# Optimization experiments

Measured on AMD Instinct MI355X. Metric: run time of the kernel, lower is better.

Reference implementation:

```python
import jax, jax.numpy as jnp
import numpy as np

N = 100000          # nodes
E = 1600000         # edges
IN_DIM = 128
HID = 64
N_CLASSES = 40
N_GAT_LAYERS = 2    # n_layers - 1
ALPHA = 0.2         # LeakyReLU slope
NEG_BIG = -9.0e15


def setup_inputs() -> dict:
    key = jax.random.key(0)
    ks = jax.random.split(key, 8)
    x = jax.random.normal(ks[0], (N, IN_DIM), dtype=jnp.float32)
    edge_index = jax.random.randint(ks[1], (2, E), 0, N, dtype=jnp.int64)
    # parameters (xavier-ish scale)
    emb_w = jax.random.normal(ks[2], (IN_DIM, HID), dtype=jnp.float32) * (1.414 / np.sqrt(IN_DIM + HID))
    emb_b = jnp.zeros((HID,), dtype=jnp.float32)
    Ws = jax.random.normal(ks[3], (N_GAT_LAYERS, HID, HID), dtype=jnp.float32) * (1.414 / np.sqrt(2 * HID))
    attn_a = jax.random.normal(ks[4], (N_GAT_LAYERS, 1, 2 * HID), dtype=jnp.float32) * (1.414 / np.sqrt(1 + 2 * HID))
    out_w = jax.random.normal(ks[5], (HID, N_CLASSES), dtype=jnp.float32) * (1.414 / np.sqrt(HID + N_CLASSES))
    out_b = jnp.zeros((N_CLASSES,), dtype=jnp.float32)
    return {"x": x, "edge_index": edge_index, "emb_w": emb_w, "emb_b": emb_b,
            "Ws": Ws, "attn_a": attn_a, "out_w": out_w, "out_b": out_b}


def _gat_conv(x, edge_src, edge_dst, W, a):
    # x: [N, d_in], W: [d_in, d_out], a: [1, 2*d_out]
    wh = x @ W                                   # [N, d_out]
    d = wh.shape[1]
    a_src = a[0, :d]                             # [d]
    a_dst = a[0, d:]                             # [d]
    # (a * cat(wh[src], wh[dst])).sum(1) == (wh @ a_src)[src] + (wh @ a_dst)[dst]
    s_src = wh @ a_src                           # [N]
    s_dst = wh @ a_dst                           # [N]
    e = jax.nn.leaky_relu(s_src[edge_src] + s_dst[edge_dst], negative_slope=ALPHA)  # [E]
    att = jnp.where(e > 0, e, NEG_BIG)
    att = jax.nn.softmax(att, axis=0)            # GLOBAL softmax over all edges (as in source)
    # scatter-aggregate weighted neighbor features into destination nodes
    msgs = att[:, None] * wh[edge_src]           # [E, d_out]
    h_prime = jax.ops.segment_sum(msgs, edge_dst, num_segments=wh.shape[0])  # [N, d_out]
    return jax.nn.elu(h_prime)                   # concat=True branch


def reference(x, edge_index, emb_w, emb_b, Ws, attn_a, out_w, out_b):
    edge_src = edge_index[0]
    edge_dst = edge_index[1]
    h = x @ emb_w + emb_b                        # emb Linear
    for l in range(N_GAT_LAYERS):
        h = _gat_conv(h, edge_src, edge_dst, Ws[l], attn_a[l])
    h = h @ out_w + out_b                        # out_att Linear
    h = jax.nn.elu(h)
    return jax.nn.log_softmax(h, axis=1)
```

## Files before the change

kernel.cpp:

```cpp
#include <hip/hip_runtime.h>
#include <hip/hip_bf16.h>

#define NODES   100000
#define EDGES   1600000
#define INDIM   128
#define HID     64
#define NCLS    40
#define NEG_BIG_F (-9000000000000000.0f)
#define SENTINEL  (-3.0e38f)

#define BN       512
#define NBUCK    196
#define CHUNK    7168
#define NCHUNK   ((EDGES + CHUNK - 1) / CHUNK)
#define BCAP     8960
#define AGB      3125
#define SMB      128

using bf16x8 = __attribute__((ext_vector_type(8))) short;
using f32x4  = __attribute__((ext_vector_type(4))) float;

static __device__ __forceinline__ float b2f(__hip_bfloat16 h){
    return __bfloat162float(h);
}
static __device__ __forceinline__ float bits2f(unsigned int b){
    union { unsigned int u; float f; } v; v.u = b << 16; return v.f;
}
static __device__ __forceinline__ unsigned short f2b(float f){
    __hip_bfloat16 h = __float2bfloat16(f);
    return *reinterpret_cast<unsigned short*>(&h);
}
static __device__ __forceinline__ float ldin(const void* p, int i, bool f32){
    return f32 ? ((const float*)p)[i] : b2f(((const __hip_bfloat16*)p)[i]);
}
static __device__ __forceinline__ float elu_fast(float x){
    return (x > 0.f) ? x : (__expf(x) - 1.f);
}
static __device__ __forceinline__ unsigned fenc(float f){
    unsigned u = __float_as_uint(f);
    return (u & 0x80000000u) ? ~u : (u | 0x80000000u);
}
static __device__ __forceinline__ float fdec(unsigned k){
    return __uint_as_float((k & 0x80000000u) ? (k & 0x7fffffffu) : ~k);
}
static __device__ __forceinline__ int ld_src(const int* ei, int i, bool i64){
    return i64 ? ei[2*i] : ei[i];
}
static __device__ __forceinline__ int ld_dst(const int* ei, int i, bool i64){
    return i64 ? ei[2*(EDGES + i)] : ei[EDGES + i];
}

__global__ __launch_bounds__(256) void k_detect(const unsigned* __restrict__ xw,
                                                const unsigned* __restrict__ eiw,
                                                int* __restrict__ flags){
    __shared__ int s1[256], s2[256];
    int t = threadIdx.x;
    int c1 = 0, c2 = 0;
    for(int i = t; i < 1024; i += 256){
        unsigned e = (xw[i] >> 23) & 0xffu;
        c1 += (e >= 90u && e <= 160u) ? 1 : 0;
        c2 += (eiw[2*i + 1] == 0u) ? 1 : 0;
    }
    s1[t] = c1; s2[t] = c2; __syncthreads();
    for(int off = 128; off > 0; off >>= 1){
        if(t < off){ s1[t] += s1[t+off]; s2[t] += s2[t+off]; }
        __syncthreads();
    }
    if(t == 0){ flags[0] = (s1[0] > 512) ? 1 : 0; flags[1] = (s2[0] > 512) ? 1 : 0; }
}

__global__ __launch_bounds__(256) void k_bhist(const int* __restrict__ ei,
                                               const int* __restrict__ flags,
                                               int* __restrict__ bdeg){
    __shared__ int sh[NBUCK];
    bool i64 = flags[1] != 0;
    int t = threadIdx.x;
    for(int i = t; i < NBUCK; i += 256) sh[i] = 0;
    __syncthreads();
    int i = blockIdx.x*256 + t;
    int stride = gridDim.x*256;
    for(; i < EDGES; i += stride) atomicAdd(&sh[ld_dst(ei, i, i64) >> 9], 1);
    __syncthreads();
    for(int b = t; b < NBUCK; b += 256) if(sh[b]) atomicAdd(&bdeg[b], sh[b]);
}

__global__ __launch_bounds__(256) void k_bscan(const int* __restrict__ bdeg,
                        int* __restrict__ bstart, int* __restrict__ bcursor,
                        unsigned* __restrict__ maxk){
    __shared__ int sh[256];
    int t = threadIdx.x;
    int v = (t < NBUCK) ? bdeg[t] : 0;
    sh[t] = v; __syncthreads();
    for(int off = 1; off < 256; off <<= 1){
        int x = (t >= off) ? sh[t - off] : 0;
        __syncthreads();
        sh[t] += x;
        __syncthreads();
    }
    int excl = sh[t] - v;
    if(t < NBUCK){ bstart[t] = excl; bcursor[t] = excl; }
    if(t == 255) bstart[NBUCK] = sh[255];
    if(t == 0){ maxk[0] = 0u; maxk[1] = 0u; }
}

__global__ __launch_bounds__(256) void k_bucket_scatter(const int* __restrict__ ei,
    const int* __restrict__ flags, int* __restrict__ bcursor, int* __restrict__ tmp){
    __shared__ int  sCnt[NBUCK], sScan[NBUCK], sCur[NBUCK], sGofs[NBUCK];
    __shared__ int  stage[CHUNK];
    __shared__ unsigned char bId[CHUNK];
    bool i64 = flags[1] != 0;
    int t = threadIdx.x;
    int base = blockIdx.x * CHUNK;
    int n = EDGES - base; if(n > CHUNK) n = CHUNK; if(n <= 0) return;

    for(int b = t; b < NBUCK; b += 256) sCnt[b] = 0;
    __syncthreads();
    for(int j = t; j < n; j += 256)
        atomicAdd(&sCnt[ld_dst(ei, base + j, i64) >> 9], 1);
    __syncthreads();
    for(int b = t; b < NBUCK; b += 256) sScan[b] = sCnt[b];
    __syncthreads();
    for(int off = 1; off < NBUCK; off <<= 1){
        int v = 0;
        if(t < NBUCK && t >= off) v = sScan[t - off];
        __syncthreads();
        if(t < NBUCK) sScan[t] += v;
        __syncthreads();
    }
    if(t < NBUCK){
        int excl = sScan[t] - sCnt[t];
        sCur[t]  = excl;
        sGofs[t] = sCnt[t] ? atomicAdd(&bcursor[t], sCnt[t]) : 0;
    }
    __syncthreads();
    for(int j = t; j < n; j += 256){
        int src = ld_src(ei, base + j, i64);
        int dst = ld_dst(ei, base + j, i64);
        int b   = dst >> 9;
        int pos = atomicAdd(&sCur[b], 1);
        stage[pos] = src | ((dst & 511) << 17);
        bId[pos]   = (unsigned char)b;
    }
    __syncthreads();
    for(int i = t; i < n; i += 256){
        int e = stage[i];
        int b = bId[i];
        int excl = sScan[b] - sCnt[b];
        tmp[(size_t)sGofs[b] + (i - excl)] = e;
    }
}

__global__ __launch_bounds__(512) void k_bucket_sort(const int* __restrict__ tmp,
    const int* __restrict__ bstart, int* __restrict__ col,
    int* __restrict__ rowst){
    __shared__ int sCnt[BN], sScan[BN], sCur[BN];
    __shared__ int stage[BCAP];
    int b = blockIdx.x, t = threadIdx.x;
    int nb0 = b * BN;
    int gbase = bstart[b], gend = bstart[b+1];
    int cnt = gend - gbase;

    if(t < BN) sCnt[t] = 0;
    __syncthreads();
    for(int j = gbase + t; j < gend; j += 512)
        atomicAdd(&sCnt[tmp[j] >> 17], 1);
    __syncthreads();
    if(t < BN) sScan[t] = sCnt[t];
    __syncthreads();
    for(int off = 1; off < BN; off <<= 1){
        int v = 0;
        if(t < BN && t >= off) v = sScan[t - off];
        __syncthreads();
        if(t < BN) sScan[t] += v;
        __syncthreads();
    }
    if(t < BN) sCur[t] = sScan[t] - sCnt[t];
    if(t < BN && (nb0 + t) < NODES) rowst[nb0 + t] = gbase + (sScan[t] - sCnt[t]);
    if(b == 0 && t == 0) rowst[NODES] = EDGES;
    __syncthreads();
    for(int j = gbase + t; j < gend; j += 512){
        int e = tmp[j];
        int pos = atomicAdd(&sCur[e >> 17], 1);
        if(pos < BCAP) stage[pos] = e;
        else col[gbase + pos] = e & 0x1FFFF;
    }
    __syncthreads();
    int lim = (cnt < BCAP) ? cnt : BCAP;
    for(int i = t; i < lim; i += 512)
        col[gbase + i] = stage[i] & 0x1FFFF;
}

template<int K, int AMODE, bool WITH_BIAS, bool WITH_SCORES, bool CBF16, int SCALEA>
__global__ __launch_bounds__(256) void k_gemm(
    const void* __restrict__ Aptr,
    const void* __restrict__ Wb,   int woff,
    const void* __restrict__ biasb,
    const void* __restrict__ attnb, int aoff,
    const int*  __restrict__ flags,
    void* __restrict__ Cout,
    float* __restrict__ s_src,
    float* __restrict__ s_dst,
    const float* __restrict__ sdstv,
    const float2* __restrict__ MZg)
{
    __shared__ short As[64][72];
    __shared__ short Bs[64][72];
    const bool wf32 = flags[0] != 0;
    const bool af32 = (AMODE == 2) ? true : ((AMODE == 3) ? false : wf32);
    const int t = threadIdx.x;
    const int block_row = blockIdx.x * 64;
    const int w  = t >> 6;
    const int l  = t & 63;
    const int srow = t >> 2;
    const int sq   = t & 3;
    const int grow_s = block_row + srow;

    float sA = 1.f;
    if constexpr (SCALEA == 1){
        float2 gz = MZg[0];
        float sd = (grow_s < NODES) ? sdstv[grow_s] : 0.f;
        sA = __expf(sd - gz.x) * gz.y;
    }

    f32x4 acc[4] = { {0.f,0.f,0.f,0.f},{0.f,0.f,0.f,0.f},
                     {0.f,0.f,0.f,0.f},{0.f,0.f,0.f,0.f} };

    for(int kb = 0; kb < K; kb += 64){
        {
            unsigned o[16];
            if(af32){
                const float4* av4 = (const float4*)((const float*)Aptr + (size_t)grow_s*K + kb);
                #pragma unroll
                for(int i=0;i<4;i++){
                    float4 u = make_float4(0.f,0.f,0.f,0.f);
                    if(grow_s < NODES) u = av4[sq*4 + i];
                    if constexpr (SCALEA == 1){
                        u.x = elu_fast(u.x*sA); u.y = elu_fast(u.y*sA);
                        u.z = elu_fast(u.z*sA); u.w = elu_fast(u.w*sA);
                    }
                    o[4*i+0]=f2b(u.x); o[4*i+1]=f2b(u.y);
                    o[4*i+2]=f2b(u.z); o[4*i+3]=f2b(u.w);
                }
            } else {
                const uint4* avb = (const uint4*)((const unsigned short*)Aptr + (size_t)grow_s*K + kb);
                #pragma unroll
                for(int i=0;i<2;i++){
                    uint4 u = make_uint4(0,0,0,0);
                    if(grow_s < NODES) u = avb[sq*2 + i];
                    unsigned raw[8] = {u.x&0xffffu, u.x>>16, u.y&0xffffu, u.y>>16,
                                       u.z&0xffffu, u.z>>16, u.w&0xffffu, u.w>>16};
                    if constexpr (SCALEA == 1){
                        #pragma unroll
                        for(int j=0;j<8;j++) raw[j] = f2b(elu_fast(bits2f(raw[j])*sA));
                    }
                    #pragma unroll
                    for(int j=0;j<8;j++) o[8*i+j] = raw[j];
                }
            }
            uint4* dst = (uint4*)&As[srow][sq*16];
            dst[0] = make_uint4(o[0]|(o[1]<<16),  o[2]|(o[3]<<16),
                                o[4]|(o[5]<<16),  o[6]|(o[7]<<16));
            dst[1] = make_uint4(o[8]|(o[9]<<16),  o[10]|(o[11]<<16),
                                o[12]|(o[13]<<16),o[14]|(o[15]<<16));
        }
        if(wf32){
            const float* wv = (const float*)Wb + woff + (size_t)kb*64;
            #pragma unroll
            for(int i=0;i<16;i++){
                int idx = t + 256*i;
                Bs[idx & 63][idx >> 6] = (short)f2b(wv[idx]);
            }
        } else {
            const unsigned short* wv = (const unsigned short*)Wb + woff + (size_t)kb*64;
            #pragma unroll
            for(int i=0;i<16;i++){
                int idx = t + 256*i;
                Bs[idx & 63][idx >> 6] = (short)wv[idx];
            }
        }
        __syncthreads();
        #pragma unroll
        for(int s=0;s<2;s++){
            int k0 = s*32 + 8*(l >> 4);
            bf16x8 a = *(const bf16x8*)&As[16*w + (l & 15)][k0];
            #pragma unroll
            for(int c=0;c<4;c++){
                bf16x8 b = *(const bf16x8*)&Bs[16*c + (l & 15)][k0];
                acc[c] = __builtin_amdgcn_mfma_f32_16x16x32_bf16(a, b, acc[c], 0, 0, 0);
            }
        }
        __syncthreads();
    }

    const int lg4 = (l >> 4) * 4;
    const int lc  = l & 15;
    float bias[4] = {0.f,0.f,0.f,0.f};
    if constexpr (WITH_BIAS){
        #pragma unroll
        for(int c=0;c<4;c++) bias[c] = ldin(biasb, 16*c + lc, wf32);
    }
    #pragma unroll
    for(int r=0;r<4;r++){
        int grow = block_row + 16*w + lg4 + r;
        if(grow < NODES){
            #pragma unroll
            for(int c=0;c<4;c++){
                float vv = acc[c][r] + bias[c];
                if constexpr (CBF16)
                    ((unsigned short*)Cout)[(size_t)grow*64 + 16*c + lc] = f2b(vv);
                else
                    ((float*)Cout)[(size_t)grow*64 + 16*c + lc] = vv;
            }
        }
    }
    if constexpr (WITH_SCORES){
        float as_[4], ad_[4];
        #pragma unroll
        for(int c=0;c<4;c++){
            as_[c] = ldin(attnb, aoff + 16*c + lc, wf32);
            ad_[c] = ldin(attnb, aoff + 64 + 16*c + lc, wf32);
        }
        #pragma unroll
        for(int r=0;r<4;r++){
            float ps = 0.f, pd = 0.f;
            #pragma unroll
            for(int c=0;c<4;c++){
                ps = fmaf(acc[c][r], as_[c], ps);
                pd = fmaf(acc[c][r], ad_[c], pd);
            }
            ps += __shfl_xor(ps, 1, 64); pd += __shfl_xor(pd, 1, 64);
            ps += __shfl_xor(ps, 2, 64); pd += __shfl_xor(pd, 2, 64);
            ps += __shfl_xor(ps, 4, 64); pd += __shfl_xor(pd, 4, 64);
            ps += __shfl_xor(ps, 8, 64); pd += __shfl_xor(pd, 8, 64);
            int grow = block_row + 16*w + lg4 + r;
            if(lc == 0 && grow < NODES){ s_src[grow] = ps; s_dst[grow] = pd; }
        }
    }
}

__global__ __launch_bounds__(256) void k_smax(const float* __restrict__ ssrc,
                                              const float* __restrict__ sdst,
                                              unsigned* __restrict__ smaxk,
                                              unsigned* __restrict__ dmaxk){
    int tid = blockIdx.x*256 + threadIdx.x;
    int stride = gridDim.x*256;
    float m1 = SENTINEL, m2 = SENTINEL;
    for(int i = tid; i < NODES; i += stride){
        m1 = fmaxf(m1, ssrc[i]);
        m2 = fmaxf(m2, sdst[i]);
    }
    #pragma unroll
    for(int off=1; off<64; off<<=1){
        m1 = fmaxf(m1, __shfl_xor(m1, off, 64));
        m2 = fmaxf(m2, __shfl_xor(m2, off, 64));
    }
    __shared__ float sm1[4], sm2[4];
    int w = threadIdx.x >> 6;
    if((threadIdx.x & 63) == 0){ sm1[w] = m1; sm2[w] = m2; }
    __syncthreads();
    if(threadIdx.x == 0){
        for(int i=1;i<4;i++){ m1 = fmaxf(m1, sm1[i]); m2 = fmaxf(m2, sm2[i]); }
        atomicMax(smaxk, fenc(m1));
        atomicMax(dmaxk, fenc(m2));
    }
}

__global__ __launch_bounds__(256) void k_aggregate(const unsigned short* __restrict__ wh16,
    const int* __restrict__ row_start, const int* __restrict__ col,
    const float* __restrict__ ssrc, const float* __restrict__ sdst,
    const unsigned* __restrict__ smaxk, const unsigned* __restrict__ dmaxk,
    unsigned short* __restrict__ U16, float* __restrict__ zpart)
{
    int gw = (blockIdx.x*256 + threadIdx.x) >> 3;
    int l8 = threadIdx.x & 7;
    int sb = (threadIdx.x & 63) & ~7;
    int c8 = l8 * 8;
    int beg = row_start[gw], end = row_start[gw+1];
    float sdn = sdst[gw];
    const float m = fdec(*smaxk) + sdn;
    float zl = 0.f;
    float acc[8] = {0.f,0.f,0.f,0.f,0.f,0.f,0.f,0.f};
    for(int base = beg; base < end; base += 16){
        int idx0 = base + l8;
        int idx1 = base + 8 + l8;
        bool v0 = idx0 < end, v1 = idx1 < end;
        int s0 = v0 ? col[idx0] : 0;
        int s1 = v1 ? col[idx1] : 0;
        float x0 = ssrc[s0] + sdn;
        float x1 = ssrc[s1] + sdn;
        float att0 = (v0 && x0 > 0.f) ? x0 : NEG_BIG_F;
        float att1 = (v1 && x1 > 0.f) ? x1 : NEG_BIG_F;
        float w0 = __expf(att0 - m);
        float w1 = __expf(att1 - m);
        zl += w0 + w1;
        #pragma unroll
        for(int j = 0; j < 8; j++){
            int   s = __shfl(s0, sb + j, 64);
            float a = __shfl(w0, sb + j, 64);
            uint4 u = *(const uint4*)&wh16[(size_t)s*64 + c8];
            acc[0] = fmaf(a, bits2f(u.x & 0xffffu), acc[0]);
            acc[1] = fmaf(a, bits2f(u.x >> 16),     acc[1]);
            acc[2] = fmaf(a, bits2f(u.y & 0xffffu), acc[2]);
            acc[3] = fmaf(a, bits2f(u.y >> 16),     acc[3]);
            acc[4] = fmaf(a, bits2f(u.z & 0xffffu), acc[4]);
            acc[5] = fmaf(a, bits2f(u.z >> 16),     acc[5]);
            acc[6] = fmaf(a, bits2f(u.w & 0xffffu), acc[6]);
            acc[7] = fmaf(a, bits2f(u.w >> 16),     acc[7]);
        }
        #pragma unroll
        for(int j = 0; j < 8; j++){
            int   s = __shfl(s1, sb + j, 64);
            float a = __shfl(w1, sb + j, 64);
            uint4 u = *(const uint4*)&wh16[(size_t)s*64 + c8];
            acc[0] = fmaf(a, bits2f(u.x & 0xffffu), acc[0]);
            acc[1] = fmaf(a, bits2f(u.x >> 16),     acc[1]);
            acc[2] = fmaf(a, bits2f(u.y & 0xffffu), acc[2]);
            acc[3] = fmaf(a, bits2f(u.y >> 16),     acc[3]);
            acc[4] = fmaf(a, bits2f(u.z & 0xffffu), acc[4]);
            acc[5] = fmaf(a, bits2f(u.z >> 16),     acc[5]);
            acc[6] = fmaf(a, bits2f(u.w & 0xffffu), acc[6]);
            acc[7] = fmaf(a, bits2f(u.w >> 16),     acc[7]);
        }
    }
    zl += __shfl_xor(zl, 1, 64);
    zl += __shfl_xor(zl, 2, 64);
    zl += __shfl_xor(zl, 4, 64);
    float zc = (l8 == 0) ? zl * __expf(sdn - fdec(*dmaxk)) : 0.f;
    zc += __shfl_xor(zc, 8, 64);
    zc += __shfl_xor(zc, 16, 64);
    zc += __shfl_xor(zc, 32, 64);
    __shared__ float zsh[4];
    if((threadIdx.x & 63) == 0) zsh[threadIdx.x >> 6] = zc;
    __syncthreads();
    if(threadIdx.x == 0) zpart[blockIdx.x] = zsh[0]+zsh[1]+zsh[2]+zsh[3];
    ushort4 o0 = make_ushort4(f2b(acc[0]), f2b(acc[1]), f2b(acc[2]), f2b(acc[3]));
    ushort4 o1 = make_ushort4(f2b(acc[4]), f2b(acc[5]), f2b(acc[6]), f2b(acc[7]));
    *(ushort4*)&U16[(size_t)gw*64 + c8 + 0] = o0;
    *(ushort4*)&U16[(size_t)gw*64 + c8 + 4] = o1;
}

__global__ __launch_bounds__(256) void k_zfin(const float* __restrict__ zpart,
                                              float2* __restrict__ MZ,
                                              unsigned* __restrict__ smaxk,
                                              unsigned* __restrict__ dmaxk){
    int t = threadIdx.x;
    float z = 0.f;
    for(int i = t; i < AGB; i += 256) z += zpart[i];
    #pragma unroll
    for(int off=1; off<64; off<<=1) z += __shfl_xor(z, off, 64);
    __shared__ float sz[4];
    int w = t >> 6;
    if((t & 63) == 0) sz[w] = z;
    __syncthreads();
    if(t == 0){
        z = sz[0]+sz[1]+sz[2]+sz[3];
        MZ[0] = make_float2(fdec(*dmaxk), 1.0f / z);
        smaxk[0] = 0u;
        dmaxk[0] = 0u;
    }
}

__global__ __launch_bounds__(256) void k_out(const unsigned short* __restrict__ h16,
    const float* __restrict__ sdstv, const float2* __restrict__ MZg,
    const void* __restrict__ Wo, const void* __restrict__ bo,
    const int* __restrict__ flags, float* __restrict__ out)
{
    __shared__ short As[64][72];
    __shared__ short Bs[48][72];
    __shared__ float logits[64][44];
    __shared__ float rlz[64];
    bool f32 = flags[0] != 0;
    int t = threadIdx.x;
    int block_row = blockIdx.x * 64;
    const int w = t >> 6, l = t & 63;
    const int srow = t >> 2, sq = t & 3;
    const int grow_s = block_row + srow;

    {
        float2 gz = MZg[0];
        float sd = (grow_s < NODES) ? sdstv[grow_s] : 0.f;
        float sA = __expf(sd - gz.x) * gz.y;
        unsigned o[16];
        const uint4* avb = (const uint4*)(h16 + (size_t)grow_s*64);
        #pragma unroll
        for(int i=0;i<2;i++){
            uint4 u = make_uint4(0,0,0,0);
            if(grow_s < NODES) u = avb[sq*2 + i];
            unsigned raw[8] = {u.x&0xffffu, u.x>>16, u.y&0xffffu, u.y>>16,
                               u.z&0xffffu, u.z>>16, u.w&0xffffu, u.w>>16};
            #pragma unroll
            for(int j=0;j<8;j++) o[8*i+j] = f2b(elu_fast(bits2f(raw[j])*sA));
        }
        uint4* dst = (uint4*)&As[srow][sq*16];
        dst[0] = make_uint4(o[0]|(o[1]<<16),  o[2]|(o[3]<<16),
                            o[4]|(o[5]<<16),  o[6]|(o[7]<<16));
        dst[1] = make_uint4(o[8]|(o[9]<<16),  o[10]|(o[11]<<16),
                            o[12]|(o[13]<<16),o[14]|(o[15]<<16));
    }
    for(int i = t; i < 8*64; i += 256) Bs[40 + (i>>6)][i & 63] = 0;
    for(int i = t; i < 64*NCLS; i += 256){
        int k = i / NCLS, c = i % NCLS;
        Bs[c][k] = (short)(f32 ? f2b(((const float*)Wo)[i])
                               : ((const unsigned short*)Wo)[i]);
    }
    __syncthreads();

    f32x4 acc[3] = { {0.f,0.f,0.f,0.f},{0.f,0.f,0.f,0.f},{0.f,0.f,0.f,0.f} };
    #pragma unroll
    for(int s=0;s<2;s++){
        int k0 = s*32 + 8*(l >> 4);
        bf16x8 a = *(const bf16x8*)&As[16*w + (l & 15)][k0];
        #pragma unroll
        for(int c=0;c<3;c++){
            bf16x8 b = *(const bf16x8*)&Bs[16*c + (l & 15)][k0];
            acc[c] = __builtin_amdgcn_mfma_f32_16x16x32_bf16(a, b, acc[c], 0, 0, 0);
        }
    }
    {
        const int lg4 = (l >> 4) * 4;
        const int lc  = l & 15;
        #pragma unroll
        for(int c=0;c<3;c++){
            int colv = 16*c + lc;
            if(colv < NCLS){
                float bia = ldin(bo, colv, f32);
                #pragma unroll
                for(int r=0;r<4;r++)
                    logits[16*w + lg4 + r][colv] = elu_fast(acc[c][r] + bia);
            }
        }
    }
    __syncthreads();

    {
        int r = t >> 2, qq = t & 3;
        float m = SENTINEL;
        #pragma unroll
        for(int i=0;i<10;i++) m = fmaxf(m, logits[r][qq*10 + i]);
        m = fmaxf(m, __shfl_xor(m, 1, 64));
        m = fmaxf(m, __shfl_xor(m, 2, 64));
        float s = 0.f;
        #pragma unroll
        for(int i=0;i<10;i++) s += __expf(logits[r][qq*10 + i] - m);
        s += __shfl_xor(s, 1, 64);
        s += __shfl_xor(s, 2, 64);
        if(qq == 0) rlz[r] = m + logf(s);
    }
    __syncthreads();

    for(int i = t; i < 64*NCLS; i += 256){
        int rr = i / NCLS, cc = i % NCLS;
        if(block_row + rr < NODES)
            out[(size_t)(block_row)*NCLS + i] = logits[rr][cc] - rlz[rr];
    }
}

extern "C" void kernel_launch(void* const* d_in, const int* in_sizes, int n_in,
                              void* d_out, int out_size, void* d_ws, size_t ws_size,
                              hipStream_t stream)
{
    const void* x      = d_in[0];
    const int*  ei     = (const int*)d_in[1];
    const void* emb_w  = d_in[2];
    const void* emb_b  = d_in[3];
    const void* Ws     = d_in[4];
    const void* attn_a = d_in[5];
    const void* out_w  = d_in[6];
    const void* out_b  = d_in[7];
    float* out = (float*)d_out;

    char* ws = (char*)d_ws;
    size_t off = 0;
    auto alloc = [&](size_t bytes)->char*{
        char* p = ws + off;
        off = (off + bytes + 255) & ~(size_t)255;
        return p;
    };
    int*    flags   = (int*)   alloc(256);
    unsigned short* U16  = (unsigned short*)alloc((size_t)NODES*HID*2);
    unsigned short* h0   = (unsigned short*)alloc((size_t)NODES*HID*2);
    unsigned short* wh16 = (unsigned short*)alloc((size_t)NODES*HID*2);
    float*  ssrc    = (float*) alloc((size_t)NODES*4);
    float*  sdstA   = (float*) alloc((size_t)NODES*4);
    float*  sdstB   = (float*) alloc((size_t)NODES*4);
    int*    rowst   = (int*)   alloc((size_t)(NODES+1)*4);
    int*    col     = (int*)   alloc((size_t)EDGES*4);
    int*    bdeg    = (int*)   alloc(NBUCK*4);
    int*    bstart  = (int*)   alloc((NBUCK+1)*4);
    int*    bcursor = (int*)   alloc(NBUCK*4);
    float*  zpart   = (float*) alloc(AGB*4);
    float2* MZ      = (float2*)alloc(16);
    unsigned* maxk  = (unsigned*)alloc(256);

    int* tmp = (int*)U16;

    k_detect<<<1, 256, 0, stream>>>((const unsigned*)x, (const unsigned*)ei, flags);

    hipMemsetAsync(bdeg, 0, NBUCK*4, stream);
    k_bhist<<<256, 256, 0, stream>>>(ei, flags, bdeg);
    k_bscan<<<1, 256, 0, stream>>>(bdeg, bstart, bcursor, maxk);
    k_bucket_scatter<<<NCHUNK, 256, 0, stream>>>(ei, flags, bcursor, tmp);
    k_bucket_sort<<<NBUCK, 512, 0, stream>>>(tmp, bstart, col, rowst);

    k_gemm<INDIM, 0, true, false, true, 0><<<(NODES+63)/64, 256, 0, stream>>>(
        x, emb_w, 0, emb_b, nullptr, 0, flags, h0, nullptr, nullptr, nullptr, nullptr);

    k_gemm<HID, 3, false, true, true, 0><<<(NODES+63)/64, 256, 0, stream>>>(
        h0, Ws, 0, nullptr, attn_a, 0, flags, wh16, ssrc, sdstA, nullptr, nullptr);
    k_smax<<<SMB, 256, 0, stream>>>(ssrc, sdstA, maxk, maxk+1);
    k_aggregate<<<AGB, 256, 0, stream>>>(wh16, rowst, col, ssrc, sdstA, maxk, maxk+1, U16, zpart);
    k_zfin<<<1, 256, 0, stream>>>(zpart, MZ, maxk, maxk+1);

    k_gemm<HID, 3, false, true, true, 1><<<(NODES+63)/64, 256, 0, stream>>>(
        U16, Ws, HID*HID, nullptr, attn_a, 2*HID, flags, wh16, ssrc, sdstB, sdstA, MZ);
    k_smax<<<SMB, 256, 0, stream>>>(ssrc, sdstB, maxk, maxk+1);
    k_aggregate<<<AGB, 256, 0, stream>>>(wh16, rowst, col, ssrc, sdstB, maxk, maxk+1, U16, zpart);
    k_zfin<<<1, 256, 0, stream>>>(zpart, MZ, maxk, maxk+1);

    k_out<<<(NODES+63)/64, 256, 0, stream>>>(U16, sdstB, MZ, out_w, out_b, flags, out);
}
```

Before: 293.7 us.

## Fold embedding weight into first GAT weight and fuse score max into GEMM

```diff
diff --git a/kernel.cpp b/kernel.cpp
--- a/kernel.cpp
+++ b/kernel.cpp
@@ -15,7 +15,7 @@
 #define NCHUNK   ((EDGES + CHUNK - 1) / CHUNK)
 #define BCAP     8960
 #define AGB      3125
-#define SMB      128
+#define NGB      ((NODES + 63) / 64)
 
 using bf16x8 = __attribute__((ext_vector_type(8))) short;
 using f32x4  = __attribute__((ext_vector_type(4))) float;
@@ -85,8 +85,7 @@
 }
 
 __global__ __launch_bounds__(256) void k_bscan(const int* __restrict__ bdeg,
-                        int* __restrict__ bstart, int* __restrict__ bcursor,
-                        unsigned* __restrict__ maxk){
+                        int* __restrict__ bstart, int* __restrict__ bcursor){
     __shared__ int sh[256];
     int t = threadIdx.x;
     int v = (t < NBUCK) ? bdeg[t] : 0;
@@ -100,7 +99,6 @@
     int excl = sh[t] - v;
     if(t < NBUCK){ bstart[t] = excl; bcursor[t] = excl; }
     if(t == 255) bstart[NBUCK] = sh[255];
-    if(t == 0){ maxk[0] = 0u; maxk[1] = 0u; }
 }
 
 __global__ __launch_bounds__(256) void k_bucket_scatter(const int* __restrict__ ei,
@@ -190,7 +188,34 @@
         col[gbase + i] = stage[i] & 0x1FFFF;
 }
 
-template<int K, int AMODE, bool WITH_BIAS, bool WITH_SCORES, bool CBF16, int SCALEA>
+__global__ __launch_bounds__(256) void k_wfuse(const void* __restrict__ emb_w,
+    const void* __restrict__ emb_b, const void* __restrict__ Ws,
+    const int* __restrict__ flags,
+    unsigned short* __restrict__ We16, float* __restrict__ be){
+    __shared__ float W0[64][65];
+    bool f32 = flags[0] != 0;
+    int t = threadIdx.x;
+    for(int i = t; i < 4096; i += 256)
+        W0[i >> 6][i & 63] = ldin(Ws, i, f32);
+    __syncthreads();
+    int rr = 16*blockIdx.x + (t >> 4);
+    int c0 = (t & 15) * 4;
+    float acc[4] = {0.f,0.f,0.f,0.f};
+    for(int j = 0; j < 64; j++){
+        float a = ldin(emb_w, rr*64 + j, f32);
+        #pragma unroll
+        for(int c=0;c<4;c++) acc[c] = fmaf(a, W0[j][c0+c], acc[c]);
+    }
+    #pragma unroll
+    for(int c=0;c<4;c++) We16[rr*64 + c0 + c] = f2b(acc[c]);
+    if(blockIdx.x == 0 && t < 64){
+        float s = 0.f;
+        for(int j = 0; j < 64; j++) s = fmaf(ldin(emb_b, j, f32), W0[j][t], s);
+        be[t] = s;
+    }
+}
+
+template<int K, int AMODE, bool WITH_BIAS, bool WITH_SCORES, bool CBF16, int SCALEA, int WMODE>
 __global__ __launch_bounds__(256) void k_gemm(
     const void* __restrict__ Aptr,
     const void* __restrict__ Wb,   int woff,
@@ -201,12 +226,14 @@
     float* __restrict__ s_src,
     float* __restrict__ s_dst,
     const float* __restrict__ sdstv,
-    const float2* __restrict__ MZg)
+    const float2* __restrict__ MZg,
+    float2* __restrict__ pblk)
 {
     __shared__ short As[64][72];
     __shared__ short Bs[64][72];
     const bool wf32 = flags[0] != 0;
-    const bool af32 = (AMODE == 2) ? true : ((AMODE == 3) ? false : wf32);
+    const bool af32 = (AMODE == 3) ? false : wf32;
+    const bool wbf16 = (WMODE == 3) ? true : !wf32;
     const int t = threadIdx.x;
     const int block_row = blockIdx.x * 64;
     const int w  = t >> 6;
@@ -263,7 +290,7 @@
             dst[1] = make_uint4(o[8]|(o[9]<<16),  o[10]|(o[11]<<16),
                                 o[12]|(o[13]<<16),o[14]|(o[15]<<16));
         }
-        if(wf32){
+        if(!wbf16){
             const float* wv = (const float*)Wb + woff + (size_t)kb*64;
             #pragma unroll
             for(int i=0;i<16;i++){
@@ -297,7 +324,8 @@
     float bias[4] = {0.f,0.f,0.f,0.f};
     if constexpr (WITH_BIAS){
         #pragma unroll
-        for(int c=0;c<4;c++) bias[c] = ldin(biasb, 16*c + lc, wf32);
+        for(int c=0;c<4;c++)
+            bias[c] = ldin(biasb, 16*c + lc, (WMODE == 3) ? true : wf32);
     }
     #pragma unroll
     for(int r=0;r<4;r++){
@@ -320,6 +348,7 @@
             as_[c] = ldin(attnb, aoff + 16*c + lc, wf32);
             ad_[c] = ldin(attnb, aoff + 64 + 16*c + lc, wf32);
         }
+        float pmS = SENTINEL, pmD = SENTINEL;
         #pragma unroll
         for(int r=0;r<4;r++){
             float ps = 0.f, pd = 0.f;
@@ -333,21 +362,35 @@
             ps += __shfl_xor(ps, 4, 64); pd += __shfl_xor(pd, 4, 64);
             ps += __shfl_xor(ps, 8, 64); pd += __shfl_xor(pd, 8, 64);
             int grow = block_row + 16*w + lg4 + r;
-            if(lc == 0 && grow < NODES){ s_src[grow] = ps; s_dst[grow] = pd; }
-        }
-    }
-}
-
-__global__ __launch_bounds__(256) void k_smax(const float* __restrict__ ssrc,
-                                              const float* __restrict__ sdst,
-                                              unsigned* __restrict__ smaxk,
-                                              unsigned* __restrict__ dmaxk){
-    int tid = blockIdx.x*256 + threadIdx.x;
-    int stride = gridDim.x*256;
+            if(grow < NODES){
+                pmS = fmaxf(pmS, ps);
+                pmD = fmaxf(pmD, pd);
+                if(lc == 0){ s_src[grow] = ps; s_dst[grow] = pd; }
+            }
+        }
+        pmS = fmaxf(pmS, __shfl_xor(pmS, 16, 64));
+        pmS = fmaxf(pmS, __shfl_xor(pmS, 32, 64));
+        pmD = fmaxf(pmD, __shfl_xor(pmD, 16, 64));
+        pmD = fmaxf(pmD, __shfl_xor(pmD, 32, 64));
+        __shared__ float bmS[4], bmD[4];
+        if(l == 0){ bmS[w] = pmS; bmD[w] = pmD; }
+        __syncthreads();
+        if(t == 0){
+            float S = fmaxf(fmaxf(bmS[0], bmS[1]), fmaxf(bmS[2], bmS[3]));
+            float D = fmaxf(fmaxf(bmD[0], bmD[1]), fmaxf(bmD[2], bmD[3]));
+            pblk[blockIdx.x] = make_float2(S, D);
+        }
+    }
+}
+
+__global__ __launch_bounds__(256) void k_maxfold(const float2* __restrict__ pblk,
+                                                 unsigned* __restrict__ maxk){
+    int t = threadIdx.x;
     float m1 = SENTINEL, m2 = SENTINEL;
-    for(int i = tid; i < NODES; i += stride){
-        m1 = fmaxf(m1, ssrc[i]);
-        m2 = fmaxf(m2, sdst[i]);
+    for(int i = t; i < NGB; i += 256){
+        float2 e = pblk[i];
+        m1 = fmaxf(m1, e.x);
+        m2 = fmaxf(m2, e.y);
     }
     #pragma unroll
     for(int off=1; off<64; off<<=1){
@@ -355,13 +398,13 @@
         m2 = fmaxf(m2, __shfl_xor(m2, off, 64));
     }
     __shared__ float sm1[4], sm2[4];
-    int w = threadIdx.x >> 6;
-    if((threadIdx.x & 63) == 0){ sm1[w] = m1; sm2[w] = m2; }
-    __syncthreads();
-    if(threadIdx.x == 0){
+    int w = t >> 6;
+    if((t & 63) == 0){ sm1[w] = m1; sm2[w] = m2; }
+    __syncthreads();
+    if(t == 0){
         for(int i=1;i<4;i++){ m1 = fmaxf(m1, sm1[i]); m2 = fmaxf(m2, sm2[i]); }
-        atomicMax(smaxk, fenc(m1));
-        atomicMax(dmaxk, fenc(m2));
+        maxk[0] = fenc(m1);
+        maxk[1] = fenc(m2);
     }
 }
 
@@ -441,8 +484,7 @@
 
 __global__ __launch_bounds__(256) void k_zfin(const float* __restrict__ zpart,
                                               float2* __restrict__ MZ,
-                                              unsigned* __restrict__ smaxk,
-                                              unsigned* __restrict__ dmaxk){
+                                              const unsigned* __restrict__ dmaxk){
     int t = threadIdx.x;
     float z = 0.f;
     for(int i = t; i < AGB; i += 256) z += zpart[i];
@@ -455,8 +497,6 @@
     if(t == 0){
         z = sz[0]+sz[1]+sz[2]+sz[3];
         MZ[0] = make_float2(fdec(*dmaxk), 1.0f / z);
-        smaxk[0] = 0u;
-        dmaxk[0] = 0u;
     }
 }
 
@@ -578,7 +618,6 @@
     };
     int*    flags   = (int*)   alloc(256);
     unsigned short* U16  = (unsigned short*)alloc((size_t)NODES*HID*2);
-    unsigned short* h0   = (unsigned short*)alloc((size_t)NODES*HID*2);
     unsigned short* wh16 = (unsigned short*)alloc((size_t)NODES*HID*2);
     float*  ssrc    = (float*) alloc((size_t)NODES*4);
     float*  sdstA   = (float*) alloc((size_t)NODES*4);
@@ -589,6 +628,9 @@
     int*    bstart  = (int*)   alloc((NBUCK+1)*4);
     int*    bcursor = (int*)   alloc(NBUCK*4);
     float*  zpart   = (float*) alloc(AGB*4);
+    float2* pblk    = (float2*)alloc((size_t)NGB*8);
+    unsigned short* We16 = (unsigned short*)alloc((size_t)INDIM*HID*2);
+    float*  be      = (float*) alloc(HID*4);
     float2* MZ      = (float2*)alloc(16);
     unsigned* maxk  = (unsigned*)alloc(256);
 
@@ -598,24 +640,23 @@
 
     hipMemsetAsync(bdeg, 0, NBUCK*4, stream);
     k_bhist<<<256, 256, 0, stream>>>(ei, flags, bdeg);
-    k_bscan<<<1, 256, 0, stream>>>(bdeg, bstart, bcursor, maxk);
+    k_bscan<<<1, 256, 0, stream>>>(bdeg, bstart, bcursor);
     k_bucket_scatter<<<NCHUNK, 256, 0, stream>>>(ei, flags, bcursor, tmp);
     k_bucket_sort<<<NBUCK, 512, 0, stream>>>(tmp, bstart, col, rowst);
 
-    k_gemm<INDIM, 0, true, false, true, 0><<<(NODES+63)/64, 256, 0, stream>>>(
-        x, emb_w, 0, emb_b, nullptr, 0, flags, h0, nullptr, nullptr, nullptr, nullptr);
-
-    k_gemm<HID, 3, false, true, true, 0><<<(NODES+63)/64, 256, 0, stream>>>(
-        h0, Ws, 0, nullptr, attn_a, 0, flags, wh16, ssrc, sdstA, nullptr, nullptr);
-    k_smax<<<SMB, 256, 0, stream>>>(ssrc, sdstA, maxk, maxk+1);
+    k_wfuse<<<8, 256, 0, stream>>>(emb_w, emb_b, Ws, flags, We16, be);
+
+    k_gemm<INDIM, 0, true, true, true, 0, 3><<<NGB, 256, 0, stream>>>(
+        x, We16, 0, be, attn_a, 0, flags, wh16, ssrc, sdstA, nullptr, nullptr, pblk);
+    k_maxfold<<<1, 256, 0, stream>>>(pblk, maxk);
     k_aggregate<<<AGB, 256, 0, stream>>>(wh16, rowst, col, ssrc, sdstA, maxk, maxk+1, U16, zpart);
-    k_zfin<<<1, 256, 0, stream>>>(zpart, MZ, maxk, maxk+1);
-
-    k_gemm<HID, 3, false, true, true, 1><<<(NODES+63)/64, 256, 0, stream>>>(
-        U16, Ws, HID*HID, nullptr, attn_a, 2*HID, flags, wh16, ssrc, sdstB, sdstA, MZ);
-    k_smax<<<SMB, 256, 0, stream>>>(ssrc, sdstB, maxk, maxk+1);
+    k_zfin<<<1, 256, 0, stream>>>(zpart, MZ, maxk+1);
+
+    k_gemm<HID, 3, false, true, true, 1, 0><<<NGB, 256, 0, stream>>>(
+        U16, Ws, HID*HID, nullptr, attn_a, 2*HID, flags, wh16, ssrc, sdstB, sdstA, MZ, pblk);
+    k_maxfold<<<1, 256, 0, stream>>>(pblk, maxk);
     k_aggregate<<<AGB, 256, 0, stream>>>(wh16, rowst, col, ssrc, sdstB, maxk, maxk+1, U16, zpart);
-    k_zfin<<<1, 256, 0, stream>>>(zpart, MZ, maxk, maxk+1);
-
-    k_out<<<(NODES+63)/64, 256, 0, stream>>>(U16, sdstB, MZ, out_w, out_b, flags, out);
-}
+    k_zfin<<<1, 256, 0, stream>>>(zpart, MZ, maxk+1);
+
+    k_out<<<NGB, 256, 0, stream>>>(U16, sdstB, MZ, out_w, out_b, flags, out);
+}
```

New measurement: 302.0 us. 1.03x slower.
